# Kernel tuning notes

Measured on AMD Instinct MI355X. Metric: run time of the kernel, lower is better.

Reference implementation:

```python
import jax, jax.numpy as jnp
import numpy as np

# Module constants (match init_kwargs)
G = 8        # number of channel groups (len(list_input_dim))
D = 16       # per-group input dim
L = 1024     # sequence length
B = 16       # batch
E = 8        # num_experts
OUT = 64     # out_channels
KS = 3       # emb_kernel_size
K = 4        # hardcoded self.k in Channel_Embedding
LOSS_COEF = 0.01


def setup_inputs() -> dict:
    key = jax.random.key(0)
    k0, k1, k2, k3 = jax.random.split(key, 4)
    x = jax.random.normal(k0, (B, G * D, L), jnp.float32)
    # torch inits w_gate to zeros (degenerate); use small random weights for meaningful routing
    w_gate = jax.random.normal(k1, (G, D * 5, E), jnp.float32) * 0.1
    conv1_w = jax.random.normal(k2, (G, OUT, D, KS), jnp.float32) * (1.0 / np.sqrt(D * KS))
    conv1_b = jnp.zeros((G, OUT), jnp.float32)
    conv2_w = jax.random.normal(k3, (G, OUT * E, OUT, 1), jnp.float32) * (1.0 / np.sqrt(OUT))
    conv2_b = jnp.zeros((G, OUT * E), jnp.float32)
    return dict(x=x, w_gate=w_gate, conv1_w=conv1_w, conv1_b=conv1_b,
                conv2_w=conv2_w, conv2_b=conv2_b)


def _cv_squared(v):
    # torch: x.float().var() (unbiased) / (mean^2 + eps)
    v = v.astype(jnp.float32)
    return jnp.var(v, ddof=1) / (jnp.mean(v) ** 2 + 1e-10)


def _conv1d(x, w, b):
    # x [B,C,L], w [O,I,K] -> [B,O,L'] (VALID, stride 1)
    y = jax.lax.conv_general_dilated(x, w, (1,), 'VALID',
                                     dimension_numbers=('NCH', 'OIH', 'NCH'))
    return y + b[None, :, None]


def _group_forward(xg, wg, c1w, c1b, c2w, c2b):
    # xg: [B, D, L] single channel group
    Bb = xg.shape[0]
    # gating input: last timesteps [-6:-1] -> [B, D*5]
    gate_in = xg[:, :, -6:-1].reshape(Bb, -1)
    logits = jax.nn.softmax(gate_in @ wg, axis=1)           # [B, E]
    top_v, top_i = jax.lax.top_k(logits, min(K + 1, E))     # [B, K+1]
    tkv, tki = top_v[:, :K], top_i[:, :K]
    gk = tkv / (tkv.sum(1, keepdims=True) + 1e-6)
    gates = jnp.zeros_like(logits).at[jnp.arange(Bb)[:, None], tki].set(gk)  # [B, E]
    load = (gates > 0).sum(0)                               # eval path: _gates_to_load
    loss = _cv_squared(gates.sum(0)) + _cv_squared(load)
    # experts: conv(D->OUT, k=KS) -> tanh -> conv(OUT -> OUT*E, k=1)
    h = jnp.tanh(_conv1d(xg, c1w, c1b))
    raw = _conv1d(h, c2w, c2b)                              # [B, OUT*E, L']
    Lp = raw.shape[-1]
    # channel index = d*E + e (matches torch permute+reshape(B,-1,OUT,E))
    moe = jnp.einsum('bdel,be->bdl', raw.reshape(Bb, OUT, E, Lp), gates)  # [B, OUT, L']
    return moe, loss, gates


def reference(x, w_gate, conv1_w, conv1_b, conv2_w, conv2_b):
    # split channels into G groups of D: [G, B, D, L]
    xg = x.reshape(x.shape[0], G, D, x.shape[-1]).transpose(1, 0, 2, 3)
    moe, loss, gates = jax.vmap(_group_forward)(xg, w_gate, conv1_w, conv1_b, conv2_w, conv2_b)
    combine_features = moe.transpose(1, 0, 2, 3)   # [B, G, OUT, L']
    out_loss = LOSS_COEF * loss.sum()
    gates_out = gates.transpose(1, 2, 0)           # [B, E, G]
    return combine_features, out_loss, gates_out
```

## Files before the change

### kernel.cpp

```cpp
#include <hip/hip_runtime.h>
#include <hip/hip_bf16.h>

#define NG   8
#define ND   16
#define NL   1024
#define NB   16
#define NE   8
#define NOUT 64
#define NKS  3
#define NK   4
#define NLP  1022

#define OUT_LOSS  (NB*NG*NOUT*NLP)
#define OUT_GATES (OUT_LOSS + 1)

typedef short bf16x8 __attribute__((ext_vector_type(8)));
typedef float f32x4  __attribute__((ext_vector_type(4)));

#define MFMA16(A, B, C) __builtin_amdgcn_mfma_f32_16x16x32_bf16((A), (B), (C), 0, 0, 0)

__device__ __forceinline__ float tanh_fast(float x) {
    float e = exp2f(x * 2.885390081777927f);
    return 1.0f - 2.0f / (e + 1.0f);
}

__device__ __forceinline__ unsigned fbits(float a) { return __builtin_bit_cast(unsigned, a); }
__device__ __forceinline__ float resid(float a) {
    return a - __builtin_bit_cast(float, fbits(a) & 0xFFFF0000u);
}
__device__ __forceinline__ int pack2(float a, float b) {
    return (int)((fbits(a) >> 16) | (fbits(b) & 0xFFFF0000u));
}
__device__ __forceinline__ unsigned short bfb(float v) {
    __hip_bfloat16 h = __float2bfloat16(v);
    return __builtin_bit_cast(unsigned short, h);
}
__device__ __forceinline__ float bff(unsigned short s) {
    return __builtin_bit_cast(float, ((unsigned)s) << 16);
}

__device__ __forceinline__ void compute_gates_f(
    const float* __restrict__ x, const float* __restrict__ wg,
    int g, int b, float gates[8])
{
    float gi[80];
    const float* xrow = x + (size_t)(b * 128 + g * 16) * 1024 + (1024 - 6);
    #pragma unroll
    for (int d = 0; d < 16; ++d) {
        #pragma unroll
        for (int tt = 0; tt < 5; ++tt) gi[d * 5 + tt] = xrow[d * 1024 + tt];
    }
    float lg[8];
    #pragma unroll
    for (int e = 0; e < 8; ++e) lg[e] = 0.f;
    const float* wgg = wg + g * 640;
    #pragma unroll
    for (int j = 0; j < 80; ++j) {
        const float v = gi[j];
        #pragma unroll
        for (int e = 0; e < 8; ++e) lg[e] = fmaf(v, wgg[j * 8 + e], lg[e]);
    }
    float mx = lg[0];
    #pragma unroll
    for (int e = 1; e < 8; ++e) mx = fmaxf(mx, lg[e]);
    float s = 0.f;
    #pragma unroll
    for (int e = 0; e < 8; ++e) { lg[e] = expf(lg[e] - mx); s += lg[e]; }
    const float invsm = 1.f / s;
    #pragma unroll
    for (int e = 0; e < 8; ++e) lg[e] *= invsm;

    int used = 0;
    float tv[4]; int ti[4];
    #pragma unroll
    for (int k = 0; k < 4; ++k) {
        float bv = -1.f; int be = 0;
        #pragma unroll
        for (int e = 0; e < 8; ++e) {
            if (!((used >> e) & 1) && lg[e] > bv) { bv = lg[e]; be = e; }
        }
        tv[k] = bv; ti[k] = be; used |= (1 << be);
    }
    const float s4 = tv[0] + tv[1] + tv[2] + tv[3];
    const float invs = 1.f / (s4 + 1e-6f);
    #pragma unroll
    for (int e = 0; e < 8; ++e) {
        float v = 0.f;
        #pragma unroll
        for (int k = 0; k < 4; ++k) if (ti[k] == e) v = tv[k] * invs;
        gates[e] = v;
    }
}

__global__ __launch_bounds__(256) void prep_kernel(
    const float* __restrict__ x,   const float* __restrict__ wg,
    const float* __restrict__ c1w, const float* __restrict__ c2w,
    const float* __restrict__ c2b,
    float* __restrict__ out, int4* __restrict__ weffA,
    float* __restrict__ beff, int4* __restrict__ w1fA)
{
    const int bid = blockIdx.x;
    const int t   = threadIdx.x;

    __shared__ float glds[128][8];
    __shared__ float impa[64], loda[64];
    __shared__ float lossg[8];

    if (bid < 128) {
        const int gb = bid, g = gb >> 4, b = gb & 15;
        float gt[8];
        compute_gates_f(x, wg, g, b, gt);

        const int o  = t >> 2;
        const int iq = (t & 3) * 16;
        const float* w2g = c2w + (size_t)g * 512 * 64 + (size_t)o * 8 * 64 + iq;
        float acc[16];
        #pragma unroll
        for (int q = 0; q < 16; ++q) acc[q] = 0.f;
        #pragma unroll
        for (int e = 0; e < 8; ++e) {
            const float4* src = (const float4*)(w2g + e * 64);
            #pragma unroll
            for (int q = 0; q < 4; ++q) {
                float4 v = src[q];
                acc[q*4+0] = fmaf(gt[e], v.x, acc[q*4+0]);
                acc[q*4+1] = fmaf(gt[e], v.y, acc[q*4+1]);
                acc[q*4+2] = fmaf(gt[e], v.z, acc[q*4+2]);
                acc[q*4+3] = fmaf(gt[e], v.w, acc[q*4+3]);
            }
        }
        const int mt  = o >> 4;
        const int ks  = iq >> 5;
        const int lgA = (iq & 31) >> 3;
        int4* wdst = weffA + gb * 1024 + mt * 128 + ks * 64;
        #pragma unroll
        for (int R = 0; R < 2; ++R) {
            int4 whi, wlo;
            whi.x = pack2(acc[R*8+0], acc[R*8+1]);
            whi.y = pack2(acc[R*8+2], acc[R*8+3]);
            whi.z = pack2(acc[R*8+4], acc[R*8+5]);
            whi.w = pack2(acc[R*8+6], acc[R*8+7]);
            wlo.x = pack2(resid(acc[R*8+0]), resid(acc[R*8+1]));
            wlo.y = pack2(resid(acc[R*8+2]), resid(acc[R*8+3]));
            wlo.z = pack2(resid(acc[R*8+4]), resid(acc[R*8+5]));
            wlo.w = pack2(resid(acc[R*8+6]), resid(acc[R*8+7]));
            const int slot = (lgA + R) * 16 + (o & 15);
            wdst[slot]       = whi;
            wdst[512 + slot] = wlo;
        }
        if (t < 64) {
            const float* b2g = c2b + g * 512;
            float a = 0.f;
            #pragma unroll
            for (int e = 0; e < 8; ++e) a = fmaf(gt[e], b2g[t * 8 + e], a);
            beff[gb * 64 + t] = a;
        }
    } else if (bid < 136) {
        const int g = bid - 128;
        for (int u = t; u < 1024; u += 256) {
            const int s    = u >> 9;
            const int mt   = (u >> 7) & 3;
            const int ks   = (u >> 6) & 1;
            const int lgrp = (u >> 4) & 3;
            const int m    = u & 15;
            const int o    = mt * 16 + m;
            float v[8];
            #pragma unroll
            for (int e = 0; e < 8; ++e) {
                const int k = ks * 32 + lgrp * 8 + e;
                if (k < 48) {
                    const int tap = (k < 32) ? (k >> 4) : 2;
                    const int i   = k & 15;
                    const float w = c1w[((size_t)(g * 64 + o) * 16 + i) * 3 + tap];
                    v[e] = (s == 0) ? w : resid(w);
                } else v[e] = 0.f;
            }
            int4 pk;
            pk.x = pack2(v[0], v[1]); pk.y = pack2(v[2], v[3]);
            pk.z = pack2(v[4], v[5]); pk.w = pack2(v[6], v[7]);
            w1fA[(size_t)g * 1024 + u] = pk;
        }
    } else {
        float gates[8];
        const int g = t >> 4, b = t & 15;
        if (t < 128) {
            compute_gates_f(x, wg, g, b, gates);
            #pragma unroll
            for (int e = 0; e < 8; ++e) {
                glds[t][e] = gates[e];
                out[OUT_GATES + (b * 8 + e) * 8 + g] = gates[e];
            }
        }
        __syncthreads();
        if (t < 64) {
            const int gg = t >> 3, e = t & 7;
            float si = 0.f, sl = 0.f;
            for (int bb = 0; bb < 16; ++bb) {
                const float v = glds[gg * 16 + bb][e];
                si += v;
                sl += (v > 0.f) ? 1.f : 0.f;
            }
            impa[t] = si; loda[t] = sl;
        }
        __syncthreads();
        if (t < 8) {
            float m1 = 0.f, m2 = 0.f;
            #pragma unroll
            for (int e = 0; e < 8; ++e) { m1 += impa[t * 8 + e]; m2 += loda[t * 8 + e]; }
            m1 *= 0.125f; m2 *= 0.125f;
            float v1 = 0.f, v2 = 0.f;
            #pragma unroll
            for (int e = 0; e < 8; ++e) {
                const float d1 = impa[t * 8 + e] - m1, d2 = loda[t * 8 + e] - m2;
                v1 += d1 * d1; v2 += d2 * d2;
            }
            v1 *= (1.f / 7.f); v2 *= (1.f / 7.f);
            lossg[t] = v1 / (m1 * m1 + 1e-10f) + v2 / (m2 * m2 + 1e-10f);
        }
        __syncthreads();
        if (t == 0) {
            float tot = 0.f;
            #pragma unroll
            for (int gg = 0; gg < 8; ++gg) tot += lossg[gg];
            out[OUT_LOSS] = 0.01f * tot;
        }
    }
}

__global__ __launch_bounds__(256, 4) void main_kernel(
    const float* __restrict__ x,    const int4* __restrict__ w1fA,
    const float* __restrict__ b1,   const int4* __restrict__ weffA,
    const float* __restrict__ beff, float* __restrict__ out)
{
    __shared__ int4 hfrag[1024];
    __shared__ char xs[130 * 80 + 16];

    const int bid  = blockIdx.x;
    const int xcd  = bid & 7;
    const int jj   = bid >> 3;
    const int gb   = ((jj & 15) << 3) | xcd;
    const int tile = jj >> 4;
    const int g    = gb >> 4, b = gb & 15;
    const int t    = threadIdx.x;
    const int lane = t & 63;
    const int wv   = t >> 6;
    const int col  = lane & 15;
    const int j4   = lane >> 4;
    const int l0   = tile * 128;
    const int wb   = wv * 256;

    {
        const int si  = t >> 4;
        const int sc0 = t & 15;
        const float* xr = x + (size_t)(b * 128 + g * 16 + si) * 1024;
        const int boff = (si >> 3) * 32 + (si & 7) * 2;
        #pragma unroll
        for (int kk = 0; kk < 9; ++kk) {
            const int c = sc0 + kk * 16;
            if (c < 130) {
                int gc = l0 + c; if (gc > 1023) gc = 1023;
                const float v = xr[gc];
                const unsigned short hs = bfb(v);
                const unsigned short ls = bfb(v - bff(hs));
                *(unsigned short*)(xs + c * 80 + boff)      = hs;
                *(unsigned short*)(xs + c * 80 + boff + 16) = ls;
            }
        }
    }
    __syncthreads();

    const int4*  w1base = w1fA + g * 1024 + lane;
    const int4*  wAbase = weffA + gb * 1024 + lane;
    const int    rbase  = j4 << 2;
    float* outg = out + (size_t)((b * 8 + g) * 64) * NLP;

    #pragma unroll
    for (int tl = 0; tl < 2; ++tl) {
        const int nloc = (wv * 2 + tl) * 16 + col;
        bf16x8 xBh0, xBl0, xBh1, xBl1;
        {
            const char* p0 = xs + (nloc + (j4 >> 1)) * 80 + (j4 & 1) * 32;
            int4 bh = *(const int4*)p0;
            int4 bl = *(const int4*)(p0 + 16);
            xBh0 = __builtin_bit_cast(bf16x8, bh);
            xBl0 = __builtin_bit_cast(bf16x8, bl);
            const char* p1 = xs + (nloc + 2) * 80 + (j4 & 1) * 32;
            int4 ch_ = *(const int4*)p1;
            int4 cl_ = *(const int4*)(p1 + 16);
            if (j4 >= 2) {
                ch_.x = ch_.y = ch_.z = ch_.w = 0;
                cl_.x = cl_.y = cl_.z = cl_.w = 0;
            }
            xBh1 = __builtin_bit_cast(bf16x8, ch_);
            xBl1 = __builtin_bit_cast(bf16x8, cl_);
        }

        f32x4 acc1[4];
        #pragma unroll
        for (int mt = 0; mt < 4; ++mt)
            acc1[mt] = *(const f32x4*)(b1 + g * 64 + mt * 16 + rbase);
        #pragma unroll
        for (int mt = 0; mt < 4; ++mt) {
            bf16x8 Ah0 = *(const bf16x8*)(w1base + mt * 128);
            bf16x8 Ah1 = *(const bf16x8*)(w1base + mt * 128 + 64);
            bf16x8 Al0 = *(const bf16x8*)(w1base + 512 + mt * 128);
            bf16x8 Al1 = *(const bf16x8*)(w1base + 512 + mt * 128 + 64);
            f32x4 a = acc1[mt];
            a = MFMA16(Ah0, xBh0, a);
            a = MFMA16(Ah0, xBl0, a);
            a = MFMA16(Al0, xBh0, a);
            a = MFMA16(Ah1, xBh1, a);
            a = MFMA16(Ah1, xBl1, a);
            a = MFMA16(Al1, xBh1, a);
            acc1[mt] = a;
        }

        {
            char* base = (char*)hfrag;
            const int woff = (j4 & 1) * 8;
            const int lgt0 = j4 >> 1;
            #pragma unroll
            for (int mt = 0; mt < 4; ++mt) {
                const float t0 = tanh_fast(acc1[mt][0]);
                const float t1 = tanh_fast(acc1[mt][1]);
                const float t2 = tanh_fast(acc1[mt][2]);
                const float t3 = tanh_fast(acc1[mt][3]);
                const unsigned short h0 = bfb(t0), h1 = bfb(t1);
                const unsigned short h2 = bfb(t2), h3 = bfb(t3);
                uint2 whi, wlo;
                whi.x = (unsigned)h0 | ((unsigned)h1 << 16);
                whi.y = (unsigned)h2 | ((unsigned)h3 << 16);
                wlo.x = (unsigned)bfb(t0 - bff(h0)) | ((unsigned)bfb(t1 - bff(h1)) << 16);
                wlo.y = (unsigned)bfb(t2 - bff(h2)) | ((unsigned)bfb(t3 - bff(h3)) << 16);
                const int kst = mt >> 1;
                const int lgt = ((mt & 1) << 1) + lgt0;
                const int u   = wb + kst * 64 + lgt * 16 + col;
                *(uint2*)(base + u * 16 + woff)           = whi;
                *(uint2*)(base + (u + 128) * 16 + woff)   = wlo;
            }
        }

        f32x4 acc2[4];
        #pragma unroll
        for (int mt = 0; mt < 4; ++mt)
            acc2[mt] = *(const f32x4*)(beff + gb * 64 + mt * 16 + rbase);
        #pragma unroll
        for (int ks = 0; ks < 2; ++ks) {
            bf16x8 Bh = *(const bf16x8*)&hfrag[wb + ks * 64 + lane];
            bf16x8 Bl = *(const bf16x8*)&hfrag[wb + 128 + ks * 64 + lane];
            #pragma unroll
            for (int mt = 0; mt < 4; ++mt) {
                bf16x8 Ah = *(const bf16x8*)(wAbase + mt * 128 + ks * 64);
                bf16x8 Al = *(const bf16x8*)(wAbase + 512 + mt * 128 + ks * 64);
                f32x4 a = acc2[mt];
                a = MFMA16(Ah, Bh, a);
                a = MFMA16(Ah, Bl, a);
                a = MFMA16(Al, Bh, a);
                acc2[mt] = a;
            }
        }

        const int cg = l0 + nloc;
        if (cg < NLP) {
            #pragma unroll
            for (int mt = 0; mt < 4; ++mt) {
                float* orow = outg + (size_t)(mt * 16 + rbase) * NLP + cg;
                orow[0]             = acc2[mt][0];
                orow[(size_t)NLP]   = acc2[mt][1];
                orow[(size_t)NLP*2] = acc2[mt][2];
                orow[(size_t)NLP*3] = acc2[mt][3];
            }
        }
    }
}

extern "C" void kernel_launch(void* const* d_in, const int* in_sizes, int n_in,
                              void* d_out, int out_size, void* d_ws, size_t ws_size,
                              hipStream_t stream) {
    const float* x   = (const float*)d_in[0];
    const float* wg  = (const float*)d_in[1];
    const float* c1w = (const float*)d_in[2];
    const float* c1b = (const float*)d_in[3];
    const float* c2w = (const float*)d_in[4];
    const float* c2b = (const float*)d_in[5];
    float* out = (float*)d_out;

    char* ws    = (char*)d_ws;
    int4* weffA = (int4*)ws;
    int4* w1fA  = weffA + 131072;
    float* beff = (float*)(w1fA + 8192);

    prep_kernel<<<137, 256, 0, stream>>>(x, wg, c1w, c2w, c2b, out, weffA, beff, w1fA);
    main_kernel<<<1024, 256, 0, stream>>>(x, w1fA, c1b, weffA, beff, out);
}
```

Measured before the change: 113.2 us.

## Process both column tiles together to reuse weight fragments and interleave MFMAs

The main kernel now loads the conv1 and effective-weight fragments once and applies them to both 16-column tiles per wave, instead of reloading them in each of two sequential iterations. It interleaves the independent MFMA chains of the two tiles to hide MFMA latency, and hoists the bias loads to before the x staging. Shared memory is reduced by aliasing the x staging buffer with the second h-fragment buffer, which needs an extra barrier after the x fragments are read into registers. The cost is higher register pressure from the doubled accumulators and fragments, which could lower occupancy under launch_bounds(256,4).

```diff
diff --git a/kernel.cpp b/kernel.cpp
--- a/kernel.cpp
+++ b/kernel.cpp
@@ -232,8 +232,9 @@
     const float* __restrict__ b1,   const int4* __restrict__ weffA,
     const float* __restrict__ beff, float* __restrict__ out)
 {
-    __shared__ int4 hfrag[1024];
-    __shared__ char xs[130 * 80 + 16];
+    __shared__ int4 hfrag0[1024];
+    __shared__ int4 regionB[1024];
+    char* xs = (char*)regionB;
 
     const int bid  = blockIdx.x;
     const int xcd  = bid & 7;
@@ -249,6 +250,14 @@
     const int l0   = tile * 128;
     const int wb   = wv * 256;
 
+    const int rbase = j4 << 2;
+    f32x4 b1v[4], befv[4];
+    #pragma unroll
+    for (int mt = 0; mt < 4; ++mt) {
+        b1v[mt]  = *(const f32x4*)(b1 + g * 64 + mt * 16 + rbase);
+        befv[mt] = *(const f32x4*)(beff + gb * 64 + mt * 16 + rbase);
+    }
+
     {
         const int si  = t >> 4;
         const int sc0 = t & 15;
@@ -269,62 +278,63 @@
     }
     __syncthreads();
 
-    const int4*  w1base = w1fA + g * 1024 + lane;
-    const int4*  wAbase = weffA + gb * 1024 + lane;
-    const int    rbase  = j4 << 2;
-    float* outg = out + (size_t)((b * 8 + g) * 64) * NLP;
-
+    bf16x8 xBh0[2], xBl0[2], xBh1[2], xBl1[2];
+    int nloc[2];
     #pragma unroll
     for (int tl = 0; tl < 2; ++tl) {
-        const int nloc = (wv * 2 + tl) * 16 + col;
-        bf16x8 xBh0, xBl0, xBh1, xBl1;
-        {
-            const char* p0 = xs + (nloc + (j4 >> 1)) * 80 + (j4 & 1) * 32;
-            int4 bh = *(const int4*)p0;
-            int4 bl = *(const int4*)(p0 + 16);
-            xBh0 = __builtin_bit_cast(bf16x8, bh);
-            xBl0 = __builtin_bit_cast(bf16x8, bl);
-            const char* p1 = xs + (nloc + 2) * 80 + (j4 & 1) * 32;
-            int4 ch_ = *(const int4*)p1;
-            int4 cl_ = *(const int4*)(p1 + 16);
-            if (j4 >= 2) {
-                ch_.x = ch_.y = ch_.z = ch_.w = 0;
-                cl_.x = cl_.y = cl_.z = cl_.w = 0;
-            }
-            xBh1 = __builtin_bit_cast(bf16x8, ch_);
-            xBl1 = __builtin_bit_cast(bf16x8, cl_);
-        }
-
-        f32x4 acc1[4];
-        #pragma unroll
-        for (int mt = 0; mt < 4; ++mt)
-            acc1[mt] = *(const f32x4*)(b1 + g * 64 + mt * 16 + rbase);
-        #pragma unroll
-        for (int mt = 0; mt < 4; ++mt) {
-            bf16x8 Ah0 = *(const bf16x8*)(w1base + mt * 128);
-            bf16x8 Ah1 = *(const bf16x8*)(w1base + mt * 128 + 64);
-            bf16x8 Al0 = *(const bf16x8*)(w1base + 512 + mt * 128);
-            bf16x8 Al1 = *(const bf16x8*)(w1base + 512 + mt * 128 + 64);
-            f32x4 a = acc1[mt];
-            a = MFMA16(Ah0, xBh0, a);
-            a = MFMA16(Ah0, xBl0, a);
-            a = MFMA16(Al0, xBh0, a);
-            a = MFMA16(Ah1, xBh1, a);
-            a = MFMA16(Ah1, xBl1, a);
-            a = MFMA16(Al1, xBh1, a);
-            acc1[mt] = a;
-        }
-
-        {
-            char* base = (char*)hfrag;
-            const int woff = (j4 & 1) * 8;
-            const int lgt0 = j4 >> 1;
+        nloc[tl] = (wv * 2 + tl) * 16 + col;
+        const char* p0 = xs + (nloc[tl] + (j4 >> 1)) * 80 + (j4 & 1) * 32;
+        int4 bh = *(const int4*)p0;
+        int4 bl = *(const int4*)(p0 + 16);
+        xBh0[tl] = __builtin_bit_cast(bf16x8, bh);
+        xBl0[tl] = __builtin_bit_cast(bf16x8, bl);
+        const char* p1 = xs + (nloc[tl] + 2) * 80 + (j4 & 1) * 32;
+        int4 ch_ = *(const int4*)p1;
+        int4 cl_ = *(const int4*)(p1 + 16);
+        if (j4 >= 2) {
+            ch_.x = ch_.y = ch_.z = ch_.w = 0;
+            cl_.x = cl_.y = cl_.z = cl_.w = 0;
+        }
+        xBh1[tl] = __builtin_bit_cast(bf16x8, ch_);
+        xBl1[tl] = __builtin_bit_cast(bf16x8, cl_);
+    }
+    __syncthreads();
+
+    const int4* w1base = w1fA + g * 1024 + lane;
+    f32x4 acc1[2][4];
+    #pragma unroll
+    for (int mt = 0; mt < 4; ++mt) { acc1[0][mt] = b1v[mt]; acc1[1][mt] = b1v[mt]; }
+    #pragma unroll
+    for (int mt = 0; mt < 4; ++mt) {
+        bf16x8 Ah0 = *(const bf16x8*)(w1base + mt * 128);
+        bf16x8 Ah1 = *(const bf16x8*)(w1base + mt * 128 + 64);
+        bf16x8 Al0 = *(const bf16x8*)(w1base + 512 + mt * 128);
+        bf16x8 Al1 = *(const bf16x8*)(w1base + 512 + mt * 128 + 64);
+        #pragma unroll
+        for (int tl = 0; tl < 2; ++tl) {
+            f32x4 a = acc1[tl][mt];
+            a = MFMA16(Ah0, xBh0[tl], a);
+            a = MFMA16(Ah0, xBl0[tl], a);
+            a = MFMA16(Al0, xBh0[tl], a);
+            a = MFMA16(Ah1, xBh1[tl], a);
+            a = MFMA16(Ah1, xBl1[tl], a);
+            a = MFMA16(Al1, xBh1[tl], a);
+            acc1[tl][mt] = a;
+        }
+    }
+
+    {
+        const int woff = (j4 & 1) * 8;
+        const int lgt0 = j4 >> 1;
+        #pragma unroll
+        for (int tl = 0; tl < 2; ++tl) {
+            char* base = (tl == 0) ? (char*)hfrag0 : (char*)regionB;
             #pragma unroll
             for (int mt = 0; mt < 4; ++mt) {
-                const float t0 = tanh_fast(acc1[mt][0]);
-                const float t1 = tanh_fast(acc1[mt][1]);
-                const float t2 = tanh_fast(acc1[mt][2]);
-                const float t3 = tanh_fast(acc1[mt][3]);
+                const float t0 = tanh_fast(acc1[tl][mt][0]);
+                const float t1 = tanh_fast(acc1[tl][mt][1]);
+                const float t2 = tanh_fast(acc1[tl][mt][2]);
+                const float t3 = tanh_fast(acc1[tl][mt][3]);
                 const unsigned short h0 = bfb(t0), h1 = bfb(t1);
                 const unsigned short h2 = bfb(t2), h3 = bfb(t3);
                 uint2 whi, wlo;
@@ -335,40 +345,51 @@
                 const int kst = mt >> 1;
                 const int lgt = ((mt & 1) << 1) + lgt0;
                 const int u   = wb + kst * 64 + lgt * 16 + col;
-                *(uint2*)(base + u * 16 + woff)           = whi;
-                *(uint2*)(base + (u + 128) * 16 + woff)   = wlo;
-            }
-        }
-
-        f32x4 acc2[4];
-        #pragma unroll
-        for (int mt = 0; mt < 4; ++mt)
-            acc2[mt] = *(const f32x4*)(beff + gb * 64 + mt * 16 + rbase);
-        #pragma unroll
-        for (int ks = 0; ks < 2; ++ks) {
-            bf16x8 Bh = *(const bf16x8*)&hfrag[wb + ks * 64 + lane];
-            bf16x8 Bl = *(const bf16x8*)&hfrag[wb + 128 + ks * 64 + lane];
-            #pragma unroll
-            for (int mt = 0; mt < 4; ++mt) {
-                bf16x8 Ah = *(const bf16x8*)(wAbase + mt * 128 + ks * 64);
-                bf16x8 Al = *(const bf16x8*)(wAbase + 512 + mt * 128 + ks * 64);
-                f32x4 a = acc2[mt];
-                a = MFMA16(Ah, Bh, a);
-                a = MFMA16(Ah, Bl, a);
-                a = MFMA16(Al, Bh, a);
-                acc2[mt] = a;
-            }
-        }
-
-        const int cg = l0 + nloc;
+                *(uint2*)(base + u * 16 + woff)         = whi;
+                *(uint2*)(base + (u + 128) * 16 + woff) = wlo;
+            }
+        }
+    }
+
+    const int4* wAbase = weffA + gb * 1024 + lane;
+    f32x4 acc2[2][4];
+    #pragma unroll
+    for (int mt = 0; mt < 4; ++mt) { acc2[0][mt] = befv[mt]; acc2[1][mt] = befv[mt]; }
+    #pragma unroll
+    for (int ks = 0; ks < 2; ++ks) {
+        bf16x8 Bh0t = *(const bf16x8*)&hfrag0[wb + ks * 64 + lane];
+        bf16x8 Bl0t = *(const bf16x8*)&hfrag0[wb + 128 + ks * 64 + lane];
+        bf16x8 Bh1t = *(const bf16x8*)&regionB[wb + ks * 64 + lane];
+        bf16x8 Bl1t = *(const bf16x8*)&regionB[wb + 128 + ks * 64 + lane];
+        #pragma unroll
+        for (int mt = 0; mt < 4; ++mt) {
+            bf16x8 Ah = *(const bf16x8*)(wAbase + mt * 128 + ks * 64);
+            bf16x8 Al = *(const bf16x8*)(wAbase + 512 + mt * 128 + ks * 64);
+            f32x4 a0 = acc2[0][mt];
+            f32x4 a1 = acc2[1][mt];
+            a0 = MFMA16(Ah, Bh0t, a0);
+            a1 = MFMA16(Ah, Bh1t, a1);
+            a0 = MFMA16(Ah, Bl0t, a0);
+            a1 = MFMA16(Ah, Bl1t, a1);
+            a0 = MFMA16(Al, Bh0t, a0);
+            a1 = MFMA16(Al, Bh1t, a1);
+            acc2[0][mt] = a0;
+            acc2[1][mt] = a1;
+        }
+    }
+
+    float* outg = out + (size_t)((b * 8 + g) * 64) * NLP;
+    #pragma unroll
+    for (int tl = 0; tl < 2; ++tl) {
+        const int cg = l0 + nloc[tl];
         if (cg < NLP) {
             #pragma unroll
             for (int mt = 0; mt < 4; ++mt) {
                 float* orow = outg + (size_t)(mt * 16 + rbase) * NLP + cg;
-                orow[0]             = acc2[mt][0];
-                orow[(size_t)NLP]   = acc2[mt][1];
-                orow[(size_t)NLP*2] = acc2[mt][2];
-                orow[(size_t)NLP*3] = acc2[mt][3];
+                orow[0]             = acc2[tl][mt][0];
+                orow[(size_t)NLP]   = acc2[tl][mt][1];
+                orow[(size_t)NLP*2] = acc2[tl][mt][2];
+                orow[(size_t)NLP*3] = acc2[tl][mt][3];
             }
         }
     }
```

New measurement: 109.0 us. -3.7%, faster.
